# Kernel tuning notes

Hardware: AMD Instinct MI355X
Metric: run time of the kernel (lower is better)

## Reference

```python
import jax, jax.numpy as jnp
import numpy as np

# --- hyperparameters (match init_kwargs / torch defaults) ---
BLOCK_SIZE = 11
MAX_DISP = 48
CONF_TH = 0.3
DS = 2
ALPHA = 0.85          # photometric SSIM weight
GT_TH = 2.0           # GT anchor threshold
SIGN_W, MAG_W = 0.3, 0.7
W_GT, W_PHOTO, W_SIGNMAG, W_SMOOTH = 1.0, 1.0, 0.5, 0.1


def _avg_pool(x, k, stride, pad):
    # torch F.avg_pool2d with count_include_pad=True (default): zero-padded sum / k^2
    s = jax.lax.reduce_window(x, 0.0, jax.lax.add, (1, 1, k, k), (1, 1, stride, stride),
                              ((0, 0), (0, 0), (pad, pad), (pad, pad)))
    return s / (k * k)


def _ssim(x, y):
    C1, C2 = 0.01 ** 2, 0.03 ** 2
    p = lambda t: _avg_pool(t, 3, 1, 1)
    mx, my = p(x), p(y)
    sx = jnp.maximum(p(x * x) - mx * mx, 0.0)
    sy = jnp.maximum(p(y * y) - my * my, 0.0)
    sxy = p(x * y) - mx * my
    n = (2 * mx * my + C1) * (2 * sxy + C2)
    d = (mx * mx + my * my + C1) * (sx + sy + C2)
    return jnp.clip((1 - n / d) / 2, 0.0, 1.0)


def _gt_anchor(pred, gt, conf, occ):
    pos = (gt > GT_TH).astype(pred.dtype)
    trust = conf * occ * pos
    return (trust * jnp.abs(pred - gt)).sum() / jnp.maximum(trust.sum(), 1.0)


def _photometric(disp, left, right):
    B, C, H, W = left.shape
    xb = jnp.arange(W, dtype=disp.dtype)[None, None, None, :]
    xs = xb - disp                                   # sampling x coord (grid_sample, align_corners=True)
    xc = jnp.clip(xs, 0.0, W - 1.0)                  # padding_mode='border'
    x0 = jnp.floor(xc)
    w = xc - x0
    x0i = x0.astype(jnp.int32)
    x1i = jnp.minimum(x0i + 1, W - 1)
    gather = lambda idx: jnp.take_along_axis(right, jnp.broadcast_to(idx, (B, C, H, W)), axis=3)
    warped = gather(x0i) * (1.0 - w) + gather(x1i) * w   # y grid is identity under align_corners
    valid = ((xs > 0) & (xs < W - 1)).astype(disp.dtype)
    l1 = jnp.abs(left - warped).mean(axis=1, keepdims=True)
    ss = _ssim(left, warped).mean(axis=1, keepdims=True)
    err = ALPHA * ss + (1.0 - ALPHA) * l1
    return (err * valid).sum() / jnp.maximum(valid.sum(), 1.0)


def _compute_ncc_disp(left, right):
    B, C, Ho, Wo = left.shape
    lg = _avg_pool(left, DS, DS, 0).mean(axis=1, keepdims=True)   # half-res grayscale
    rg = _avg_pool(right, DS, DS, 0).mean(axis=1, keepdims=True)
    H, W = lg.shape[2], lg.shape[3]
    md = MAX_DISP // DS
    bs, pad = BLOCK_SIZE, BLOCK_SIZE // 2
    p = lambda t: _avg_pool(t, bs, 1, pad)
    lm = p(lg)
    ls = jnp.sqrt(jnp.maximum(p(lg * lg) - lm * lm, 1e-8))
    best_c = jnp.full((B, 1, H, W), -1.0, dtype=jnp.float32)
    best_d = jnp.zeros((B, 1, H, W), dtype=jnp.float32)
    for d in range(-md, md + 1):          # fixed small set of shift offsets
        if d == 0:
            continue
        if d > 0:
            rs = jnp.pad(rg[:, :, :, d:], ((0, 0), (0, 0), (0, 0), (0, d)))
        else:
            rs = jnp.pad(rg[:, :, :, :W + d], ((0, 0), (0, 0), (0, 0), (-d, 0)))
        rm = p(rs)
        rstd = jnp.sqrt(jnp.maximum(p(rs * rs) - rm * rm, 1e-8))
        cross = p(lg * rs)
        ncc = (cross - lm * rm) / (ls * rstd + 1e-8)
        better = ncc > best_c
        best_c = jnp.where(better, ncc, best_c)
        best_d = jnp.where(better, jnp.float32(d), best_d)
    nd = best_d * float(DS)
    nc = jnp.maximum(best_c, 0.0)
    # nearest upsample back to full res (exact integer factor)
    nd = jnp.repeat(jnp.repeat(nd, DS, axis=2), DS, axis=3)
    nc = jnp.repeat(jnp.repeat(nc, DS, axis=2), DS, axis=3)
    nc = nc * (nc > CONF_TH).astype(nc.dtype)
    return jax.lax.stop_gradient(nd), jax.lax.stop_gradient(nc)   # torch @no_grad


def _sign_magnitude(pred, left, right):
    nd, nc = _compute_ncc_disp(left, right)
    active = (nc > 0).astype(pred.dtype)
    n = jnp.maximum(active.sum(), 1.0)
    sign_map = jnp.sign(nd) * active
    l_sign = (jnp.maximum(-pred * sign_map, 0.0) * active).sum() / n
    l_mag = (nc * jnp.abs(pred - nd) * active).sum() / n
    return SIGN_W * l_sign + MAG_W * l_mag


def _smoothness(disp, img):
    ddx = jnp.abs(disp[:, :, :, 1:] - disp[:, :, :, :-1])
    ddy = jnp.abs(disp[:, :, 1:, :] - disp[:, :, :-1, :])
    idx = jnp.abs(img[:, :, :, 1:] - img[:, :, :, :-1]).mean(axis=1, keepdims=True)
    idy = jnp.abs(img[:, :, 1:, :] - img[:, :, :-1, :]).mean(axis=1, keepdims=True)
    return (ddx * jnp.exp(-idx)).mean() + (ddy * jnp.exp(-idy)).mean()


def _total_loss(pred, gt, conf, occ, left, right):
    return (W_GT * _gt_anchor(pred, gt, conf, occ)
            + W_PHOTO * _photometric(pred, left, right)
            + W_SIGNMAG * _sign_magnitude(pred, left, right)
            + W_SMOOTH * _smoothness(pred, left))


def setup_inputs() -> dict:
    key = jax.random.key(0)
    k = jax.random.split(key, 6)
    B, H, W = 4, 544, 960
    return {
        "pred_disp": jax.random.normal(k[0], (B, 1, H, W), dtype=jnp.float32) * 8.0,
        "gt_disp": jax.random.uniform(k[1], (B, 1, H, W), dtype=jnp.float32) * 20.0,
        "gt_conf": jax.random.uniform(k[2], (B, 1, H, W), dtype=jnp.float32),
        "gt_occ": jax.random.uniform(k[3], (B, 1, H, W), dtype=jnp.float32),
        "left_img": jax.random.uniform(k[4], (B, 3, H, W), dtype=jnp.float32),
        "right_img": jax.random.uniform(k[5], (B, 3, H, W), dtype=jnp.float32),
    }


def reference(pred_disp, gt_disp, gt_conf, gt_occ, left_img, right_img):
    return _total_loss(pred_disp, gt_disp, gt_conf, gt_occ, left_img, right_img)
```

## Files before the change

kernel.cpp:

```cpp
#include <hip/hip_runtime.h>
#include <hip/hip_bf16.h>

constexpr int B  = 4;
constexpr int H  = 544;
constexpr int W  = 960;
constexpr int H2 = 272;
constexpr int W2 = 480;
constexpr int NH = B * H2 * W2;
constexpr int NF = B * H * W;

constexpr int TPW = 32, TPH = 8;
constexpr int SW = TPW + 2, SH = TPH + 2;
constexpr int NSTAGE = SW * SH;
constexpr int GX = W / TPW;
constexpr int GY = H / TPH;
constexpr int NBLK  = GX * GY * B;
constexpr int NBLK2 = (NH + 255) / 256;

__device__ inline float waveSum(float v) {
  #pragma unroll
  for (int off = 32; off > 0; off >>= 1) v += __shfl_down(v, off, 64);
  return v;
}

__global__ __launch_bounds__(256) void k_pix(const float* __restrict__ pred,
                                             const float* __restrict__ gt,
                                             const float* __restrict__ conf,
                                             const float* __restrict__ occ,
                                             const float* __restrict__ left,
                                             const float* __restrict__ right,
                                             float* __restrict__ lg,
                                             float* __restrict__ rg,
                                             float* __restrict__ partialsA) {
  const int bx = blockIdx.x % GX;
  const int by = (blockIdx.x / GX) % GY;
  const int b  = blockIdx.x / (GX * GY);
  const int x0 = bx * TPW, y0 = by * TPH;
  const int tid = threadIdx.x;

  const float* dispb = pred + (size_t)b * H * W;
  const float* lb = left  + (size_t)b * 3 * H * W;
  const float* rb = right + (size_t)b * 3 * H * W;

  __shared__ float4 L4s[NSTAGE];
  __shared__ float4 W4s[NSTAGE];

  for (int e = tid; e < NSTAGE; e += 256) {
    int r = e / SW, c = e % SW;
    int yy = y0 - 1 + r, xx = x0 - 1 + c;
    float4 l4 = make_float4(0.f, 0.f, 0.f, 0.f);
    float4 w4 = make_float4(0.f, 0.f, 0.f, 0.f);
    if (yy >= 0 && yy < H && xx >= 0 && xx < W) {
      float dv = dispb[yy * W + xx];
      float xsv = (float)xx - dv;
      float xc = fminf(fmaxf(xsv, 0.f), (float)(W - 1));
      float x0f = floorf(xc);
      float w = xc - x0f;
      int x0i = (int)x0f;
      int x1i = min(x0i + 1, W - 1);
      const float* l0 = lb + (size_t)yy * W;
      const float* r0 = rb + (size_t)yy * W;
      l4.x = l0[xx];
      l4.y = l0[(size_t)H * W + xx];
      l4.z = l0[2 * (size_t)H * W + xx];
      l4.w = dv;
      w4.x = r0[x0i] * (1.f - w) + r0[x1i] * w;
      w4.y = r0[(size_t)H * W + x0i] * (1.f - w) + r0[(size_t)H * W + x1i] * w;
      w4.z = r0[2 * (size_t)H * W + x0i] * (1.f - w) + r0[2 * (size_t)H * W + x1i] * w;
    }
    L4s[e] = l4; W4s[e] = w4;
  }
  __syncthreads();

  if (tid < 64) {
    int hx = tid & 15, hy = tid >> 4;
    int y2g = (y0 >> 1) + hy, x2g = (x0 >> 1) + hx;
    int i00 = (2 * hy + 1) * SW + (2 * hx + 1);
    float4 a00 = L4s[i00], a01 = L4s[i00 + 1], a10 = L4s[i00 + SW], a11 = L4s[i00 + SW + 1];
    float sl = 0.f;
    sl += a00.x + a01.x + a10.x + a11.x;
    sl += a00.y + a01.y + a10.y + a11.y;
    sl += a00.z + a01.z + a10.z + a11.z;
    float sr = 0.f;
    int yy2 = y0 + 2 * hy, xx2 = x0 + 2 * hx;
    #pragma unroll
    for (int c = 0; c < 3; c++) {
      const float* rp = rb + (size_t)(c * H + yy2) * W + xx2;
      sr += rp[0] + rp[1] + rp[W] + rp[W + 1];
    }
    size_t ho = (size_t)b * (H2 * W2) + (size_t)y2g * W2 + x2g;
    lg[ho] = sl * (1.f / 12.f);
    rg[ho] = sr * (1.f / 12.f);
  }

  float v[6];
  #pragma unroll
  for (int s = 0; s < 6; s++) v[s] = 0.f;

  {
    const int tx = tid & 31, ty = tid >> 5;
    const int x = x0 + tx, y = y0 + ty;
    const size_t gidx = (size_t)b * H * W + (size_t)y * W + x;
    const int ci = (ty + 1) * SW + (tx + 1);

    float sl[3] = {0,0,0}, sw[3] = {0,0,0}, sl2[3] = {0,0,0},
          sw2[3] = {0,0,0}, slw[3] = {0,0,0};
    float4 cl4, cw4, rl4, dl4;
    #pragma unroll
    for (int dy = -1; dy <= 1; dy++) {
      #pragma unroll
      for (int dx = -1; dx <= 1; dx++) {
        int ni = ci + dy * SW + dx;
        float4 a = L4s[ni];
        float4 wv = W4s[ni];
        sl[0] += a.x;  sl2[0] += a.x * a.x;  sw[0] += wv.x;  sw2[0] += wv.x * wv.x;  slw[0] += a.x * wv.x;
        sl[1] += a.y;  sl2[1] += a.y * a.y;  sw[1] += wv.y;  sw2[1] += wv.y * wv.y;  slw[1] += a.y * wv.y;
        sl[2] += a.z;  sl2[2] += a.z * a.z;  sw[2] += wv.z;  sw2[2] += wv.z * wv.z;  slw[2] += a.z * wv.z;
        if (dy == 0 && dx == 0) { cl4 = a; cw4 = wv; }
        if (dy == 0 && dx == 1) rl4 = a;
        if (dy == 1 && dx == 0) dl4 = a;
      }
    }
    float ds = cl4.w;

    {
      float g = gt[gidx];
      float trust = (g > 2.0f) ? conf[gidx] * occ[gidx] : 0.f;
      v[0] = trust * fabsf(ds - g);
      v[1] = trust;
    }

    {
      float xs = (float)x - ds;
      bool valid = (xs > 0.f) && (xs < (float)(W - 1));
      float cl[3] = {cl4.x, cl4.y, cl4.z};
      float cw[3] = {cw4.x, cw4.y, cw4.z};
      float ssm = 0.f, l1m = 0.f;
      #pragma unroll
      for (int c = 0; c < 3; c++) {
        float mx = sl[c] * (1.f / 9.f), my = sw[c] * (1.f / 9.f);
        float sx = fmaxf(sl2[c] * (1.f / 9.f) - mx * mx, 0.f);
        float sy = fmaxf(sw2[c] * (1.f / 9.f) - my * my, 0.f);
        float sxy = slw[c] * (1.f / 9.f) - mx * my;
        float n  = (2.f * mx * my + 1e-4f) * (2.f * sxy + 9e-4f);
        float dd = (mx * mx + my * my + 1e-4f) * (sx + sy + 9e-4f);
        float ss = (1.f - n / dd) * 0.5f;
        ss = fminf(fmaxf(ss, 0.f), 1.f);
        ssm += ss;
        l1m += fabsf(cl[c] - cw[c]);
      }
      ssm *= (1.f / 3.f); l1m *= (1.f / 3.f);
      float err = 0.85f * ssm + 0.15f * l1m;
      if (valid) { v[2] = err; v[3] = 1.f; }
    }

    if (x < W - 1) {
      float ddx = fabsf(rl4.w - ds);
      float idx = fabsf(rl4.x - cl4.x) + fabsf(rl4.y - cl4.y) + fabsf(rl4.z - cl4.z);
      v[4] = ddx * __expf(-idx * (1.f / 3.f));
    }
    if (y < H - 1) {
      float ddy = fabsf(dl4.w - ds);
      float idy = fabsf(dl4.x - cl4.x) + fabsf(dl4.y - cl4.y) + fabsf(dl4.z - cl4.z);
      v[5] = ddy * __expf(-idy * (1.f / 3.f));
    }
  }

  __shared__ float sm[4][6];
  int wave = threadIdx.x >> 6, lane = threadIdx.x & 63;
  #pragma unroll
  for (int s = 0; s < 6; s++) {
    float r = waveSum(v[s]);
    if (lane == 0) sm[wave][s] = r;
  }
  __syncthreads();
  if (threadIdx.x < 6) {
    float t = sm[0][threadIdx.x] + sm[1][threadIdx.x] +
              sm[2][threadIdx.x] + sm[3][threadIdx.x];
    partialsA[(size_t)threadIdx.x * NBLK + blockIdx.x] = t;
  }
}

__global__ __launch_bounds__(256) void k_ncc(const float* __restrict__ lg,
                                             const float* __restrict__ rg,
                                             float* __restrict__ bcA,
                                             float* __restrict__ bdA) {
  const int z = blockIdx.z;
  const int b = z >> 2, grp = z & 3;
  const int dmin = (grp == 0) ? -24 : ((grp == 1) ? -12 : ((grp == 2) ? 1 : 13));
  const int x0 = blockIdx.x * 64;
  const int y0 = blockIdx.y * 16;
  const int tid = threadIdx.x;

  __shared__ __align__(16) float SM[8770];
  float* LGs = SM;
  float* RMS = SM;
  float* RGs = SM + 2432;
  float* POOL = SM + 4642;
  float* P1 = SM + 7970;
  float* P2 = SM + 8370;

  const float* lgb = lg + (size_t)b * (H2 * W2);
  const float* rgb = rg + (size_t)b * (H2 * W2);

  for (int e = tid; e < 26 * 74; e += 256) {
    int r = e / 74, c = e % 74;
    int gy = y0 - 5 + r, gxx = x0 - 5 + c;
    LGs[e] = (gy >= 0 && gy < H2 && gxx >= 0 && gxx < W2) ? lgb[gy * W2 + gxx] : 0.f;
  }
  const int col0RG = x0 - 5 + dmin;
  for (int e = tid; e < 26 * 85; e += 256) {
    int r = e / 85, c = e % 85;
    int gy = y0 - 5 + r, gxx = col0RG + c;
    RGs[e] = (gy >= 0 && gy < H2 && gxx >= 0 && gxx < W2) ? rgb[gy * W2 + gxx] : 0.f;
  }
  __syncthreads();

  const int hg = tid & 7, hr = tid >> 3;
  float lgc[18];
  float* LH1 = POOL;
  float* LH2 = POOL + 1664;
  if (hr < 26) {
    #pragma unroll
    for (int k = 0; k < 18; k++) lgc[k] = LGs[hr * 74 + 8 * hg + k];
    float w1[8], w2[8];
    float s1 = 0.f, s2 = 0.f;
    #pragma unroll
    for (int k = 0; k < 11; k++) { s1 += lgc[k]; s2 += lgc[k] * lgc[k]; }
    w1[0] = s1; w2[0] = s2;
    #pragma unroll
    for (int j = 1; j < 8; j++) {
      s1 += lgc[j + 10] - lgc[j - 1];
      s2 += lgc[j + 10] * lgc[j + 10] - lgc[j - 1] * lgc[j - 1];
      w1[j] = s1; w2[j] = s2;
    }
    *(float4*)&LH1[hr * 64 + 8 * hg]     = make_float4(w1[0], w1[1], w1[2], w1[3]);
    *(float4*)&LH1[hr * 64 + 8 * hg + 4] = make_float4(w1[4], w1[5], w1[6], w1[7]);
    *(float4*)&LH2[hr * 64 + 8 * hg]     = make_float4(w2[0], w2[1], w2[2], w2[3]);
    *(float4*)&LH2[hr * 64 + 8 * hg + 4] = make_float4(w2[4], w2[5], w2[6], w2[7]);
  }
  const bool headT = (grp >= 2) && (x0 == 0);
  const bool tailT = (grp < 2) && (x0 == 448);
  if (headT || tailT) {
    int gcol0 = headT ? 0 : 456;
    for (int e = tid; e < 16 * 24; e += 256) {
      int y = e / 24, i = e % 24;
      int lc = gcol0 + i - col0RG;
      float v1 = 0.f, v2 = 0.f;
      if (lc >= 0 && lc < 85) {
        #pragma unroll
        for (int dy = 0; dy < 11; dy++) {
          float v = RGs[(y + dy) * 85 + lc];
          v1 += v; v2 += v * v;
        }
      }
      P1[y * 25 + i + 1] = v1;
      P2[y * 25 + i + 1] = v2;
    }
  }
  __syncthreads();

  if ((headT || tailT) && tid < 16) {
    int y = tid;
    float s1 = 0.f, s2 = 0.f;
    P1[y * 25] = 0.f; P2[y * 25] = 0.f;
    for (int k = 0; k < 24; k++) {
      s1 += P1[y * 25 + k + 1]; P1[y * 25 + k + 1] = s1;
      s2 += P2[y * 25 + k + 1]; P2[y * 25 + k + 1] = s2;
    }
  }
  const int vx = tid & 63;
  const int vys = (tid >> 6) * 4;
  float lmS[4], lsS[4];
  {
    float s1 = 0.f, s2 = 0.f;
    #pragma unroll
    for (int dy = 0; dy < 11; dy++) { s1 += LH1[(vys + dy) * 64 + vx]; s2 += LH2[(vys + dy) * 64 + vx]; }
    #pragma unroll
    for (int k = 0; k < 4; k++) {
      if (k) {
        s1 += LH1[(vys + k + 10) * 64 + vx] - LH1[(vys + k - 1) * 64 + vx];
        s2 += LH2[(vys + k + 10) * 64 + vx] - LH2[(vys + k - 1) * 64 + vx];
      }
      float m = s1 * (1.f / 121.f);
      float s = sqrtf(fmaxf(s2 * (1.f / 121.f) - m * m, 1e-8f));
      lmS[k] = m * 121.f;
      lsS[k] = s * 121.f;
    }
  }
  __syncthreads();

  float* VR1 = POOL;
  float* VR2 = POOL + 1360;
  if (tid < 170) {
    int c = tid % 85;
    int rr0 = (tid / 85) * 8;
    float s1 = 0.f, s2 = 0.f;
    #pragma unroll
    for (int dy = 0; dy < 11; dy++) {
      float v = RGs[(rr0 + dy) * 85 + c];
      s1 += v; s2 += v * v;
    }
    VR1[rr0 * 85 + c] = s1; VR2[rr0 * 85 + c] = s2;
    #pragma unroll
    for (int k = 1; k < 8; k++) {
      float vin  = RGs[(rr0 + k + 10) * 85 + c];
      float vout = RGs[(rr0 + k - 1) * 85 + c];
      s1 += vin - vout;
      s2 += vin * vin - vout * vout;
      VR1[(rr0 + k) * 85 + c] = s1; VR2[(rr0 + k) * 85 + c] = s2;
    }
  }
  __syncthreads();

  {
    int r = tid >> 4, seg = tid & 15;
    int c0 = seg * 5;
    if (c0 < 75) {
      float s1 = 0.f, s2 = 0.f;
      #pragma unroll
      for (int m = 0; m < 11; m++) { s1 += VR1[r * 85 + c0 + m]; s2 += VR2[r * 85 + c0 + m]; }
      #pragma unroll
      for (int j = 0; j < 5; j++) {
        if (j) {
          s1 += VR1[r * 85 + c0 + j + 10] - VR1[r * 85 + c0 + j - 1];
          s2 += VR2[r * 85 + c0 + j + 10] - VR2[r * 85 + c0 + j - 1];
        }
        float rm = s1 * (1.f / 121.f);
        float rstd = sqrtf(fmaxf(s2 * (1.f / 121.f) - rm * rm, 1e-8f));
        *(float2*)&RMS[r * 152 + 2 * (c0 + j)] = make_float2(rm, rstd);
      }
    }
  }
  __syncthreads();

  float* CH0 = POOL;
  float* CH1 = POOL + 1664;
  const int gx = x0 + vx;
  const bool headL = (grp >= 2) && (gx < 5);
  const bool tailL = (grp < 2) && (gx > 474);
  const bool edgeL = headL || tailL;
  float bnum[4], bden[4], bdd[4];
  #pragma unroll
  for (int k = 0; k < 4; k++) { bnum[k] = -1.f; bden[k] = 1.f; bdd[k] = 0.f; }

  for (int it = 0; it < 6; ++it) {
    const int d0 = dmin + 2 * it;
    if (hr < 26) {
      const int c0 = 8 * hg + 2 * it;
      float rgv[19];
      #pragma unroll
      for (int j = 0; j < 19; j++) rgv[j] = RGs[hr * 85 + c0 + j];
      float ca[8], cb[8];
      float sa = 0.f, sb = 0.f;
      #pragma unroll
      for (int k = 0; k < 11; k++) { sa += lgc[k] * rgv[k]; sb += lgc[k] * rgv[k + 1]; }
      ca[0] = sa; cb[0] = sb;
      #pragma unroll
      for (int j = 1; j < 8; j++) {
        sa += lgc[j + 10] * rgv[j + 10] - lgc[j - 1] * rgv[j - 1];
        sb += lgc[j + 10] * rgv[j + 11] - lgc[j - 1] * rgv[j];
        ca[j] = sa; cb[j] = sb;
      }
      *(float4*)&CH0[hr * 64 + 8 * hg]     = make_float4(ca[0], ca[1], ca[2], ca[3]);
      *(float4*)&CH0[hr * 64 + 8 * hg + 4] = make_float4(ca[4], ca[5], ca[6], ca[7]);
      *(float4*)&CH1[hr * 64 + 8 * hg]     = make_float4(cb[0], cb[1], cb[2], cb[3]);
      *(float4*)&CH1[hr * 64 + 8 * hg + 4] = make_float4(cb[4], cb[5], cb[6], cb[7]);
    }
    __syncthreads();
    {
      float a0 = 0.f, a1 = 0.f;
      #pragma unroll
      for (int dy = 0; dy < 11; dy++) { a0 += CH0[(vys + dy) * 64 + vx]; a1 += CH1[(vys + dy) * 64 + vx]; }
      #pragma unroll
      for (int k = 0; k < 4; k++) {
        if (k) {
          a0 += CH0[(vys + k + 10) * 64 + vx] - CH0[(vys + k - 1) * 64 + vx];
          a1 += CH1[(vys + k + 10) * 64 + vx] - CH1[(vys + k - 1) * 64 + vx];
        }
        #pragma unroll
        for (int h = 0; h < 2; h++) {
          int d = d0 + h;
          float cs = h ? a1 : a0;
          int rvi = vx + 2 * it + h;
          float2 ms = *(const float2*)&RMS[(vys + k) * 152 + 2 * rvi];
          float rm = ms.x, rstd = ms.y;
          if (edgeL) {
            float rs = rm * 121.f;
            float r2 = (rstd * rstd + rm * rm) * 121.f;
            int a, bI;
            if (headL) { a = max(gx - 5 + d, 0); bI = d; }
            else       { a = 24 + d; bI = min(gx + 5 + d, 479) - 455; }
            rs -= P1[(vys + k) * 25 + bI] - P1[(vys + k) * 25 + a];
            r2 -= P2[(vys + k) * 25 + bI] - P2[(vys + k) * 25 + a];
            rm = rs * (1.f / 121.f);
            rstd = sqrtf(fmaxf(r2 * (1.f / 121.f) - rm * rm, 1e-8f));
          }
          float num = __builtin_fmaf(-lmS[k], rm, cs);
          float den = __builtin_fmaf(lsS[k], rstd, 1.21e-6f);
          if (num * bden[k] > bnum[k] * den) { bnum[k] = num; bden[k] = den; bdd[k] = (float)d; }
        }
      }
    }
    __syncthreads();
  }

  if (gx < W2) {
    float* bcp = bcA + (size_t)grp * NH + (size_t)b * (H2 * W2);
    float* bdp = bdA + (size_t)grp * NH + (size_t)b * (H2 * W2);
    #pragma unroll
    for (int k = 0; k < 4; k++) {
      size_t o = (size_t)(y0 + vys + k) * W2 + gx;
      bcp[o] = bnum[k] / bden[k];
      bdp[o] = bdd[k];
    }
  }
}

__global__ __launch_bounds__(256) void k_sgm(const float* __restrict__ pred,
                                             const float* __restrict__ bcA,
                                             const float* __restrict__ bdA,
                                             float* __restrict__ partialsB) {
  int tid = blockIdx.x * 256 + threadIdx.x;
  float v6 = 0.f, v7 = 0.f, v8 = 0.f;
  if (tid < NH) {
    int b = tid / (H2 * W2);
    int rem = tid % (H2 * W2);
    int y2 = rem / W2, x2 = rem % W2;
    float bcv = bcA[tid];
    float bdv = bdA[tid];
    #pragma unroll
    for (int g = 1; g < 4; g++) {
      float c = bcA[(size_t)g * NH + tid];
      if (c > bcv) { bcv = c; bdv = bdA[(size_t)g * NH + tid]; }
    }
    if (bcv > 0.3f) {
      float nd = bdv * 2.f;
      float sgn = (nd > 0.f) ? 1.f : ((nd < 0.f) ? -1.f : 0.f);
      const float* pb = pred + (size_t)b * H * W;
      #pragma unroll
      for (int dy = 0; dy < 2; dy++) {
        #pragma unroll
        for (int dx = 0; dx < 2; dx++) {
          float p = pb[(size_t)(2 * y2 + dy) * W + 2 * x2 + dx];
          v6 += fmaxf(-p * sgn, 0.f);
          v7 += bcv * fabsf(p - nd);
        }
      }
      v8 = 4.f;
    }
  }
  __shared__ float sm[4][3];
  int wave = threadIdx.x >> 6, lane = threadIdx.x & 63;
  float r;
  r = waveSum(v6); if (lane == 0) sm[wave][0] = r;
  r = waveSum(v7); if (lane == 0) sm[wave][1] = r;
  r = waveSum(v8); if (lane == 0) sm[wave][2] = r;
  __syncthreads();
  if (threadIdx.x < 3) {
    float t = sm[0][threadIdx.x] + sm[1][threadIdx.x] +
              sm[2][threadIdx.x] + sm[3][threadIdx.x];
    partialsB[(size_t)threadIdx.x * NBLK2 + blockIdx.x] = t;
  }
}

__global__ __launch_bounds__(1024) void k_final(const float* __restrict__ PA,
                                                const float* __restrict__ PB,
                                                float* __restrict__ out) {
  __shared__ float red[9][16];
  int lane = threadIdx.x & 63, wave = threadIdx.x >> 6;
  #pragma unroll
  for (int s = 0; s < 6; s++) {
    float l = 0.f;
    for (int i = threadIdx.x; i < NBLK; i += 1024) l += PA[(size_t)s * NBLK + i];
    l = waveSum(l);
    if (lane == 0) red[s][wave] = l;
  }
  #pragma unroll
  for (int s = 0; s < 3; s++) {
    float l = 0.f;
    for (int i = threadIdx.x; i < NBLK2; i += 1024) l += PB[(size_t)s * NBLK2 + i];
    l = waveSum(l);
    if (lane == 0) red[6 + s][wave] = l;
  }
  __syncthreads();
  if (threadIdx.x == 0) {
    float a[9];
    #pragma unroll
    for (int s = 0; s < 9; s++) {
      float t = 0.f;
      #pragma unroll
      for (int q = 0; q < 16; q++) t += red[s][q];
      a[s] = t;
    }
    float gtl = a[0] / fmaxf(a[1], 1.f);
    float ph  = a[2] / fmaxf(a[3], 1.f);
    float n   = fmaxf(a[8], 1.f);
    float smv = 0.3f * (a[6] / n) + 0.7f * (a[7] / n);
    float smo = a[4] * (1.f / ((float)B * H * (W - 1)))
              + a[5] * (1.f / ((float)B * (H - 1) * W));
    out[0] = gtl + ph + 0.5f * smv + 0.1f * smo;
  }
}

extern "C" void kernel_launch(void* const* d_in, const int* in_sizes, int n_in,
                              void* d_out, int out_size, void* d_ws, size_t ws_size,
                              hipStream_t stream) {
  const float* pred  = (const float*)d_in[0];
  const float* gt    = (const float*)d_in[1];
  const float* conf  = (const float*)d_in[2];
  const float* occ   = (const float*)d_in[3];
  const float* left  = (const float*)d_in[4];
  const float* right = (const float*)d_in[5];
  float* out = (float*)d_out;

  float* ws = (float*)d_ws;
  float* lg  = ws;
  float* rg  = ws + (size_t)NH;
  float* bcA = ws + 2 * (size_t)NH;
  float* bdA = ws + 6 * (size_t)NH;
  float* partialsA = ws + 10 * (size_t)NH;
  float* partialsB = partialsA + 6 * (size_t)NBLK;

  k_pix<<<NBLK, 256, 0, stream>>>(pred, gt, conf, occ, left, right,
                                  lg, rg, partialsA);

  dim3 nccGrid(8, 17, 16);
  k_ncc<<<nccGrid, 256, 0, stream>>>(lg, rg, bcA, bdA);

  k_sgm<<<NBLK2, 256, 0, stream>>>(pred, bcA, bdA, partialsB);

  k_final<<<1, 1024, 0, stream>>>(partialsA, partialsB, out);
}
```

Baseline: 242.6 us.

## Double-buffer NCC horizontal correlation passes and cache right-image row in registers

Restructures the disparity loop in k_ncc from six two-disparity iterations, each with two barriers, into twelve single-disparity iterations. The horizontal correlation pass for the next disparity is written to the alternate buffer while the vertical pass reads the current one, so one barrier per disparity is enough. The right-image row segment is loaded once into 29 registers using float4 LDS reads, made possible by padding the row stride to 88, instead of being reloaded every iteration. It also adds a launch-bounds occupancy hint, at the cost of higher register pressure and a fully unrolled loop.

After: 427.0 us. 1.76x slower.

```diff
diff --git a/kernel.cpp b/kernel.cpp
--- a/kernel.cpp
+++ b/kernel.cpp
@@ -181,10 +181,12 @@
   }
 }
 
-__global__ __launch_bounds__(256) void k_ncc(const float* __restrict__ lg,
-                                             const float* __restrict__ rg,
-                                             float* __restrict__ bcA,
-                                             float* __restrict__ bdA) {
+constexpr int RGST = 88;
+
+__global__ __launch_bounds__(256, 4) void k_ncc(const float* __restrict__ lg,
+                                                const float* __restrict__ rg,
+                                                float* __restrict__ bcA,
+                                                float* __restrict__ bdA) {
   const int z = blockIdx.z;
   const int b = z >> 2, grp = z & 3;
   const int dmin = (grp == 0) ? -24 : ((grp == 1) ? -12 : ((grp == 2) ? 1 : 13));
@@ -192,13 +194,13 @@
   const int y0 = blockIdx.y * 16;
   const int tid = threadIdx.x;
 
-  __shared__ __align__(16) float SM[8770];
+  __shared__ __align__(16) float SM[8848];
   float* LGs = SM;
   float* RMS = SM;
   float* RGs = SM + 2432;
-  float* POOL = SM + 4642;
-  float* P1 = SM + 7970;
-  float* P2 = SM + 8370;
+  float* POOL = SM + 4720;
+  float* P1 = SM + 8048;
+  float* P2 = SM + 8448;
 
   const float* lgb = lg + (size_t)b * (H2 * W2);
   const float* rgb = rg + (size_t)b * (H2 * W2);
@@ -212,17 +214,25 @@
   for (int e = tid; e < 26 * 85; e += 256) {
     int r = e / 85, c = e % 85;
     int gy = y0 - 5 + r, gxx = col0RG + c;
-    RGs[e] = (gy >= 0 && gy < H2 && gxx >= 0 && gxx < W2) ? rgb[gy * W2 + gxx] : 0.f;
+    RGs[r * RGST + c] = (gy >= 0 && gy < H2 && gxx >= 0 && gxx < W2) ? rgb[gy * W2 + gxx] : 0.f;
   }
   __syncthreads();
 
   const int hg = tid & 7, hr = tid >> 3;
   float lgc[18];
+  float rgv[29];
   float* LH1 = POOL;
   float* LH2 = POOL + 1664;
   if (hr < 26) {
     #pragma unroll
     for (int k = 0; k < 18; k++) lgc[k] = LGs[hr * 74 + 8 * hg + k];
+    const float* rp = &RGs[hr * RGST + 8 * hg];
+    #pragma unroll
+    for (int m = 0; m < 7; m++) {
+      float4 q = *(const float4*)(rp + 4 * m);
+      rgv[4 * m] = q.x; rgv[4 * m + 1] = q.y; rgv[4 * m + 2] = q.z; rgv[4 * m + 3] = q.w;
+    }
+    rgv[28] = rp[28];
     float w1[8], w2[8];
     float s1 = 0.f, s2 = 0.f;
     #pragma unroll
@@ -250,7 +260,7 @@
       if (lc >= 0 && lc < 85) {
         #pragma unroll
         for (int dy = 0; dy < 11; dy++) {
-          float v = RGs[(y + dy) * 85 + lc];
+          float v = RGs[(y + dy) * RGST + lc];
           v1 += v; v2 += v * v;
         }
       }
@@ -298,14 +308,14 @@
     float s1 = 0.f, s2 = 0.f;
     #pragma unroll
     for (int dy = 0; dy < 11; dy++) {
-      float v = RGs[(rr0 + dy) * 85 + c];
+      float v = RGs[(rr0 + dy) * RGST + c];
       s1 += v; s2 += v * v;
     }
     VR1[rr0 * 85 + c] = s1; VR2[rr0 * 85 + c] = s2;
     #pragma unroll
     for (int k = 1; k < 8; k++) {
-      float vin  = RGs[(rr0 + k + 10) * 85 + c];
-      float vout = RGs[(rr0 + k - 1) * 85 + c];
+      float vin  = RGs[(rr0 + k + 10) * RGST + c];
+      float vout = RGs[(rr0 + k - 1) * RGST + c];
       s1 += vin - vout;
       s2 += vin * vin - vout * vout;
       VR1[(rr0 + k) * 85 + c] = s1; VR2[(rr0 + k) * 85 + c] = s2;
@@ -334,8 +344,6 @@
   }
   __syncthreads();
 
-  float* CH0 = POOL;
-  float* CH1 = POOL + 1664;
   const int gx = x0 + vx;
   const bool headL = (grp >= 2) && (gx < 5);
   const bool tailL = (grp < 2) && (gx > 474);
@@ -344,65 +352,59 @@
   #pragma unroll
   for (int k = 0; k < 4; k++) { bnum[k] = -1.f; bden[k] = 1.f; bdd[k] = 0.f; }
 
-  for (int it = 0; it < 6; ++it) {
-    const int d0 = dmin + 2 * it;
+  auto chpass = [&](int j, float* dst) {
     if (hr < 26) {
-      const int c0 = 8 * hg + 2 * it;
-      float rgv[19];
-      #pragma unroll
-      for (int j = 0; j < 19; j++) rgv[j] = RGs[hr * 85 + c0 + j];
-      float ca[8], cb[8];
-      float sa = 0.f, sb = 0.f;
-      #pragma unroll
-      for (int k = 0; k < 11; k++) { sa += lgc[k] * rgv[k]; sb += lgc[k] * rgv[k + 1]; }
-      ca[0] = sa; cb[0] = sb;
-      #pragma unroll
-      for (int j = 1; j < 8; j++) {
-        sa += lgc[j + 10] * rgv[j + 10] - lgc[j - 1] * rgv[j - 1];
-        sb += lgc[j + 10] * rgv[j + 11] - lgc[j - 1] * rgv[j];
-        ca[j] = sa; cb[j] = sb;
-      }
-      *(float4*)&CH0[hr * 64 + 8 * hg]     = make_float4(ca[0], ca[1], ca[2], ca[3]);
-      *(float4*)&CH0[hr * 64 + 8 * hg + 4] = make_float4(ca[4], ca[5], ca[6], ca[7]);
-      *(float4*)&CH1[hr * 64 + 8 * hg]     = make_float4(cb[0], cb[1], cb[2], cb[3]);
-      *(float4*)&CH1[hr * 64 + 8 * hg + 4] = make_float4(cb[4], cb[5], cb[6], cb[7]);
-    }
-    __syncthreads();
+      float ca[8];
+      float s = 0.f;
+      #pragma unroll
+      for (int k = 0; k < 11; k++) s += lgc[k] * rgv[j + k];
+      ca[0] = s;
+      #pragma unroll
+      for (int jj = 1; jj < 8; jj++) {
+        s += lgc[jj + 10] * rgv[j + jj + 10] - lgc[jj - 1] * rgv[j + jj - 1];
+        ca[jj] = s;
+      }
+      *(float4*)&dst[hr * 64 + 8 * hg]     = make_float4(ca[0], ca[1], ca[2], ca[3]);
+      *(float4*)&dst[hr * 64 + 8 * hg + 4] = make_float4(ca[4], ca[5], ca[6], ca[7]);
+    }
+  };
+
+  chpass(0, POOL);
+  __syncthreads();
+
+  #pragma unroll
+  for (int it = 0; it < 12; ++it) {
+    float* CHr = POOL + ((it & 1) ? 1664 : 0);
+    if (it < 11) chpass(it + 1, POOL + ((it & 1) ? 0 : 1664));
+    const int d = dmin + it;
     {
-      float a0 = 0.f, a1 = 0.f;
-      #pragma unroll
-      for (int dy = 0; dy < 11; dy++) { a0 += CH0[(vys + dy) * 64 + vx]; a1 += CH1[(vys + dy) * 64 + vx]; }
+      float a = 0.f;
+      #pragma unroll
+      for (int dy = 0; dy < 11; dy++) a += CHr[(vys + dy) * 64 + vx];
       #pragma unroll
       for (int k = 0; k < 4; k++) {
-        if (k) {
-          a0 += CH0[(vys + k + 10) * 64 + vx] - CH0[(vys + k - 1) * 64 + vx];
-          a1 += CH1[(vys + k + 10) * 64 + vx] - CH1[(vys + k - 1) * 64 + vx];
+        if (k) a += CHr[(vys + k + 10) * 64 + vx] - CHr[(vys + k - 1) * 64 + vx];
+        float cs = a;
+        int rvi = vx + it;
+        float2 ms = *(const float2*)&RMS[(vys + k) * 152 + 2 * rvi];
+        float rm = ms.x, rstd = ms.y;
+        if (edgeL) {
+          float rs = rm * 121.f;
+          float r2 = (rstd * rstd + rm * rm) * 121.f;
+          int a_, bI;
+          if (headL) { a_ = max(gx - 5 + d, 0); bI = d; }
+          else       { a_ = 24 + d; bI = min(gx + 5 + d, 479) - 455; }
+          rs -= P1[(vys + k) * 25 + bI] - P1[(vys + k) * 25 + a_];
+          r2 -= P2[(vys + k) * 25 + bI] - P2[(vys + k) * 25 + a_];
+          rm = rs * (1.f / 121.f);
+          rstd = sqrtf(fmaxf(r2 * (1.f / 121.f) - rm * rm, 1e-8f));
         }
-        #pragma unroll
-        for (int h = 0; h < 2; h++) {
-          int d = d0 + h;
-          float cs = h ? a1 : a0;
-          int rvi = vx + 2 * it + h;
-          float2 ms = *(const float2*)&RMS[(vys + k) * 152 + 2 * rvi];
-          float rm = ms.x, rstd = ms.y;
-          if (edgeL) {
-            float rs = rm * 121.f;
-            float r2 = (rstd * rstd + rm * rm) * 121.f;
-            int a, bI;
-            if (headL) { a = max(gx - 5 + d, 0); bI = d; }
-            else       { a = 24 + d; bI = min(gx + 5 + d, 479) - 455; }
-            rs -= P1[(vys + k) * 25 + bI] - P1[(vys + k) * 25 + a];
-            r2 -= P2[(vys + k) * 25 + bI] - P2[(vys + k) * 25 + a];
-            rm = rs * (1.f / 121.f);
-            rstd = sqrtf(fmaxf(r2 * (1.f / 121.f) - rm * rm, 1e-8f));
-          }
-          float num = __builtin_fmaf(-lmS[k], rm, cs);
-          float den = __builtin_fmaf(lsS[k], rstd, 1.21e-6f);
-          if (num * bden[k] > bnum[k] * den) { bnum[k] = num; bden[k] = den; bdd[k] = (float)d; }
-        }
-      }
-    }
-    __syncthreads();
+        float num = __builtin_fmaf(-lmS[k], rm, cs);
+        float den = __builtin_fmaf(lsS[k], rstd, 1.21e-6f);
+        if (num * bden[k] > bnum[k] * den) { bnum[k] = num; bden[k] = den; bdd[k] = (float)d; }
+      }
+    }
+    if (it < 11) __syncthreads();
   }
 
   if (gx < W2) {
```
